# Optimization experiments

Measured on AMD Instinct MI355X. Metric: run time of the kernel, lower is better.

Reference implementation:

```python
import jax, jax.numpy as jnp
import numpy as np

B, S, D = 4, 2048, 512
H, DQK, DV = 6, 64, 64
PROJ = (DQK + DQK + DV) * H  # 1152
EPS = 1e-5


def setup_inputs() -> dict:
    key = jax.random.key(0)
    ks = jax.random.split(key, 5)
    sc = 0.05
    return {
        "x": jax.random.normal(ks[0], (B, S, D), jnp.float32),
        "Wp": jax.random.normal(ks[1], (PROJ, D), jnp.float32) * sc,
        "bp": jax.random.normal(ks[2], (PROJ,), jnp.float32) * sc,
        "Wo": jax.random.normal(ks[3], (D, H * DV), jnp.float32) * sc,
        "bo": jax.random.normal(ks[4], (D,), jnp.float32) * sc,
        "gamma": jnp.ones((D,), jnp.float32),
        "beta": jnp.zeros((D,), jnp.float32),
    }


def reference(x, Wp, bp, Wo, bo, gamma, beta):
    b, s, d = x.shape
    # 1x1 Conv1d projection == pointwise linear: [b,s,d] @ [d,proj] -> [b,s,proj]
    proj = jnp.einsum("bsd,pd->bsp", x, Wp) + bp
    q, k, v = proj[..., : H * DQK], proj[..., H * DQK : 2 * H * DQK], proj[..., 2 * H * DQK :]
    # split heads -> [b,h,s,depth]
    q = q.reshape(b, s, H, DQK).transpose(0, 2, 1, 3)
    k = k.reshape(b, s, H, DQK).transpose(0, 2, 1, 3)
    v = v.reshape(b, s, H, DV).transpose(0, 2, 1, 3)
    scores = jnp.einsum("bhqd,bhkd->bhqk", q, k) / jnp.sqrt(jnp.float32(DQK))
    attn = jax.nn.softmax(scores, axis=-1)  # softmax over kv axis
    out = jnp.einsum("bhqk,bhkd->bhqd", attn, v)
    # concat heads -> [b,s,h*dv]
    concat = out.transpose(0, 2, 1, 3).reshape(b, s, H * DV)
    y = jnp.einsum("bsf,df->bsd", concat, Wo) + bo
    z = x + y
    mu = jnp.mean(z, axis=-1, keepdims=True)
    var = jnp.mean(jnp.square(z - mu), axis=-1, keepdims=True)
    return (z - mu) / jnp.sqrt(var + EPS) * gamma + beta
```

## Files before the change

### kernel.cpp

```cpp
#include <hip/hip_runtime.h>

typedef __bf16 bf16;
typedef __bf16 bf16x8 __attribute__((ext_vector_type(8)));
typedef __bf16 bf16x4 __attribute__((ext_vector_type(4)));
typedef float  f32x4  __attribute__((ext_vector_type(4)));

#define BB 4
#define SS 2048
#define DD 512
#define HH 6
#define DH 64
#define PROJ 1152
#define FF 384
#define LDK 72

__device__ __forceinline__ bool probe_fp32(const unsigned* p) {
    return p[0] == 0x3F800000u;
}

__device__ __forceinline__ float fast_exp2(float x) {
#if __has_builtin(__builtin_amdgcn_exp2f)
    return __builtin_amdgcn_exp2f(x);
#else
    return __expf(x * 0.69314718f);
#endif
}

struct CvtSrcs { const void* s[7]; };

#define CB0 524288
#define CB1 598016
#define CB2 622592
#define CB3 622736
#define CB4 622800
#define CB5 622864
#define CB6 622928

__global__ __launch_bounds__(256) void cvt_all_kernel(
    CvtSrcs srcs, bf16* __restrict__ dst, const unsigned* __restrict__ probe)
{
    const int t = blockIdx.x * 256 + threadIdx.x;
    if (t >= CB6) return;
    int seg, base;
    if      (t < CB0) { seg = 0; base = 0;   }
    else if (t < CB1) { seg = 1; base = CB0; }
    else if (t < CB2) { seg = 2; base = CB1; }
    else if (t < CB3) { seg = 3; base = CB2; }
    else if (t < CB4) { seg = 4; base = CB3; }
    else if (t < CB5) { seg = 5; base = CB4; }
    else              { seg = 6; base = CB5; }
    const int li = (t - base) * 8;
    if (probe_fp32(probe)) {
        const float* s = (const float*)srcs.s[seg] + li;
        bf16x8 o;
#pragma unroll
        for (int j = 0; j < 8; ++j) o[j] = (bf16)s[j];
        *(bf16x8*)&dst[(size_t)t * 8] = o;
    } else {
        *(bf16x8*)&dst[(size_t)t * 8] =
            *(const bf16x8*)((const bf16*)srcs.s[seg] + li);
    }
}

template<int MERGE>
__global__ __launch_bounds__(256) void gemm_bt_kernel(
    const bf16* __restrict__ A, const float* __restrict__ lpart,
    const bf16* __restrict__ B, const bf16* __restrict__ bias,
    bf16* __restrict__ Cout, int M, int N, int K)
{
    __shared__ __attribute__((aligned(16))) bf16 sA[64 * LDK];
    __shared__ __attribute__((aligned(16))) bf16 sB[128 * LDK];

    const int tid  = threadIdx.x;
    const int lane = tid & 63;
    const int wave = tid >> 6;
    const int wn = wave * 32;
    const int l15 = lane & 15;
    const int quad = lane >> 4;
    const int bm = blockIdx.x * 64;
    const int bn = blockIdx.y * 128;
    const int KT = K / 64;

    int srowA[2], srowB[4];
    const int scol = (tid & 7) << 3;
#pragma unroll
    for (int j = 0; j < 2; ++j) srowA[j] = (j * 256 + tid) >> 3;
#pragma unroll
    for (int j = 0; j < 4; ++j) srowB[j] = (j * 256 + tid) >> 3;

    const bf16* pA[2]; const bf16* pB[4];
    const float* pl0[2];
#pragma unroll
    for (int j = 0; j < 2; ++j) {
        if (MERGE) {
            int row = bm + srowA[j];
            int b = row >> 11, q = row & (SS - 1);
            pA[j]  = A + ((size_t)(b * HH) * SS + q) * DH + scol;
            pl0[j] = lpart + (size_t)(b * HH) * SS + q;
        } else {
            pA[j] = A + (size_t)(bm + srowA[j]) * K + scol;
        }
    }
#pragma unroll
    for (int j = 0; j < 4; ++j)
        pB[j] = B + (size_t)(bn + srowB[j]) * K + scol;

    bf16x8 arb[2], a1b[2], brb[4];
    float l0[2], l1[2];

    auto loadAB = [&]() {
#pragma unroll
        for (int j = 0; j < 2; ++j) {
            arb[j] = *(const bf16x8*)pA[j];
            if (MERGE) {
                a1b[j] = *(const bf16x8*)(pA[j] + (size_t)BB * HH * SS * DH);
                l0[j] = pl0[j][0];
                l1[j] = pl0[j][(size_t)BB * HH * SS];
                pA[j]  += (size_t)SS * DH;
                pl0[j] += SS;
            } else {
                pA[j] += 64;
            }
        }
#pragma unroll
        for (int j = 0; j < 4; ++j) {
            brb[j] = *(const bf16x8*)pB[j];
            pB[j] += 64;
        }
    };

    loadAB();

    const f32x4 fzero = {0.f, 0.f, 0.f, 0.f};
    f32x4 acc[4][2];
#pragma unroll
    for (int mi = 0; mi < 4; ++mi)
#pragma unroll
        for (int ni = 0; ni < 2; ++ni) acc[mi][ni] = fzero;

    for (int kt = 0; kt < KT; ++kt) {
        __syncthreads();
#pragma unroll
        for (int j = 0; j < 2; ++j) {
            if (MERGE) {
                float inv = 1.f / (l0[j] + l1[j]);
                bf16x8 m;
#pragma unroll
                for (int e = 0; e < 8; ++e)
                    m[e] = (bf16)(((float)arb[j][e] + (float)a1b[j][e]) * inv);
                *(bf16x8*)&sA[srowA[j] * LDK + scol] = m;
            } else {
                *(bf16x8*)&sA[srowA[j] * LDK + scol] = arb[j];
            }
        }
#pragma unroll
        for (int j = 0; j < 4; ++j)
            *(bf16x8*)&sB[srowB[j] * LDK + scol] = brb[j];
        __syncthreads();
        if (kt + 1 < KT) loadAB();

#pragma unroll
        for (int kk = 0; kk < 2; ++kk) {
            bf16x8 af[4], bfr[2];
#pragma unroll
            for (int i = 0; i < 4; ++i)
                af[i] = *(const bf16x8*)&sA[(i * 16 + l15) * LDK + kk * 32 + quad * 8];
#pragma unroll
            for (int i = 0; i < 2; ++i)
                bfr[i] = *(const bf16x8*)&sB[(wn + i * 16 + l15) * LDK + kk * 32 + quad * 8];
#pragma unroll
            for (int mi = 0; mi < 4; ++mi)
#pragma unroll
                for (int ni = 0; ni < 2; ++ni)
                    acc[mi][ni] = __builtin_amdgcn_mfma_f32_16x16x32_bf16(
                        af[mi], bfr[ni], acc[mi][ni], 0, 0, 0);
        }
    }

#pragma unroll
    for (int mi = 0; mi < 4; ++mi) {
        int row = bm + mi * 16 + quad * 4;
#pragma unroll
        for (int ni = 0; ni < 2; ++ni) {
            int col = bn + wn + ni * 16 + l15;
            float bv = (float)bias[col];
#pragma unroll
            for (int r = 0; r < 4; ++r)
                Cout[(size_t)(row + r) * N + col] = (bf16)(acc[mi][ni][r] + bv);
        }
    }
}

__global__ __launch_bounds__(256) void vt_kernel(
    const bf16* __restrict__ proj, bf16* __restrict__ Vt)
{
    __shared__ __attribute__((aligned(16))) bf16 lt[64 * LDK];

    const int tid = threadIdx.x;
    const int s0 = blockIdx.x * 64;
    const int bh = blockIdx.y;
    const int b = bh / HH, h = bh % HH;

#pragma unroll
    for (int i = 0; i < 2; ++i) {
        int vid = i * 256 + tid;
        int sl = vid >> 3;
        int dc = (vid & 7) << 3;
        bf16x8 v = *(const bf16x8*)&proj[
            (size_t)(b * SS + s0 + sl) * PROJ + 2 * HH * DH + h * DH + dc];
#pragma unroll
        for (int j = 0; j < 8; ++j) {
            int d = dc + j;
            lt[d * LDK + (sl ^ (((d >> 3) & 3) * 8))] = v[j];
        }
    }
    __syncthreads();

#pragma unroll
    for (int i = 0; i < 2; ++i) {
        int vid = i * 256 + tid;
        int d = vid >> 3;
        int sc = (vid & 7) << 3;
        bf16x8 v = *(const bf16x8*)&lt[d * LDK + (sc ^ (((d >> 3) & 3) * 8))];
        *(bf16x8*)&Vt[(size_t)bh * DH * SS + (size_t)d * SS + s0 + sc] = v;
    }
}

__global__ __launch_bounds__(256) void attn_kernel(
    const bf16* __restrict__ proj, const bf16* __restrict__ Vt,
    bf16* __restrict__ Opart, float* __restrict__ lpart)
{
    __shared__ __attribute__((aligned(16))) bf16 sK [64 * LDK];
    __shared__ __attribute__((aligned(16))) bf16 sVt[64 * LDK];
    __shared__ __attribute__((aligned(16))) bf16 sP [4 * 32 * LDK];

    const int tid  = threadIdx.x;
    const int lane = tid & 63;
    const int wave = tid >> 6;
    const int l15  = lane & 15;
    const int quad = lane >> 4;

    const int bh = blockIdx.y;
    const int b = bh / HH, h = bh % HH;
    const int q0 = blockIdx.x * 128;
    const int kz = blockIdx.z;
    const bf16* base = proj + (size_t)b * SS * PROJ;
    const bf16* vtb  = Vt + (size_t)bh * DH * SS;

    const int sr = tid >> 3;
    const int sc = (tid & 7) << 3;

    const float QS = 0.18033688f;
    bf16x8 qf[2][2];
#pragma unroll
    for (int g = 0; g < 2; ++g) {
        const int qrow = q0 + wave * 32 + g * 16 + l15;
#pragma unroll
        for (int ks = 0; ks < 2; ++ks) {
            qf[ks][g] = *(const bf16x8*)&base[
                (size_t)qrow * PROJ + h * DH + ks * 32 + quad * 8];
#pragma unroll
            for (int j = 0; j < 8; ++j)
                qf[ks][g][j] = (bf16)((float)qf[ks][g][j] * QS);
        }
    }

    const f32x4 fzero = {0.f, 0.f, 0.f, 0.f};
    f32x4 lacc[2] = {fzero, fzero};
    f32x4 oacc[2][4];
#pragma unroll
    for (int g = 0; g < 2; ++g)
#pragma unroll
        for (int fi = 0; fi < 4; ++fi) oacc[g][fi] = fzero;

    bf16* pw = &sP[wave * 32 * LDK];

    const int kt0 = kz * (SS / 128);
    const int kt1 = kt0 + SS / 128;

    const bf16* pk[2]; const bf16* pv[2];
#pragma unroll
    for (int i = 0; i < 2; ++i) {
        int r = i * 32 + sr;
        pk[i] = &base[(size_t)(kt0 * 64 + r) * PROJ + HH * DH + h * DH + sc];
        pv[i] = &vtb[(size_t)r * SS + kt0 * 64 + sc];
    }
    auto loadKV = [&](bf16x8 (&kr)[2], bf16x8 (&vr)[2]) {
#pragma unroll
        for (int i = 0; i < 2; ++i) {
            kr[i] = *(const bf16x8*)pk[i];
            vr[i] = *(const bf16x8*)pv[i];
            pk[i] += (size_t)64 * PROJ;
            pv[i] += 64;
        }
    };

    bf16x8 kA[2], vA[2], kB[2], vB[2];
    loadKV(kA, vA);
    loadKV(kB, vB);

    auto tile = [&](int kt, bf16x8 (&kr)[2], bf16x8 (&vr)[2]) {
        __syncthreads();
#pragma unroll
        for (int i = 0; i < 2; ++i) {
            int r = i * 32 + sr;
            *(bf16x8*)&sK [r * LDK + sc] = kr[i];
            *(bf16x8*)&sVt[r * LDK + sc] = vr[i];
        }
        __syncthreads();
        if (kt + 2 < kt1) loadKV(kr, vr);

        f32x4 st[2][4];
#pragma unroll
        for (int mi = 0; mi < 4; ++mi) {
            bf16x8 af0 = *(const bf16x8*)&sK[(mi * 16 + l15) * LDK + quad * 8];
            bf16x8 af1 = *(const bf16x8*)&sK[(mi * 16 + l15) * LDK + 32 + quad * 8];
#pragma unroll
            for (int g = 0; g < 2; ++g) {
                st[g][mi] = __builtin_amdgcn_mfma_f32_16x16x32_bf16(
                    af0, qf[0][g], fzero, 0, 0, 0);
                st[g][mi] = __builtin_amdgcn_mfma_f32_16x16x32_bf16(
                    af1, qf[1][g], st[g][mi], 0, 0, 0);
            }
        }

#pragma unroll
        for (int g = 0; g < 2; ++g)
#pragma unroll
            for (int mi = 0; mi < 4; ++mi) {
#pragma unroll
                for (int r = 0; r < 4; ++r)
                    st[g][mi][r] = fast_exp2(st[g][mi][r]);
                lacc[g] += st[g][mi];
            }

#pragma unroll
        for (int g = 0; g < 2; ++g)
#pragma unroll
            for (int mi = 0; mi < 4; ++mi) {
                bf16x4 p4;
#pragma unroll
                for (int r = 0; r < 4; ++r) p4[r] = (bf16)st[g][mi][r];
                *(bf16x4*)&pw[(g * 16 + l15) * LDK + mi * 16 + quad * 4] = p4;
            }

#pragma unroll
        for (int ks = 0; ks < 2; ++ks) {
            bf16x8 bfrag[2];
#pragma unroll
            for (int g = 0; g < 2; ++g)
                bfrag[g] = *(const bf16x8*)&pw[(g * 16 + l15) * LDK + ks * 32 + quad * 8];
#pragma unroll
            for (int fi = 0; fi < 4; ++fi) {
                bf16x8 af = *(const bf16x8*)&sVt[(fi * 16 + l15) * LDK + ks * 32 + quad * 8];
#pragma unroll
                for (int g = 0; g < 2; ++g)
                    oacc[g][fi] = __builtin_amdgcn_mfma_f32_16x16x32_bf16(
                        af, bfrag[g], oacc[g][fi], 0, 0, 0);
            }
        }
    };

    for (int kt = kt0; kt < kt1; kt += 2) {
        tile(kt,     kA, vA);
        tile(kt + 1, kB, vB);
    }

    float l_part[2];
#pragma unroll
    for (int g = 0; g < 2; ++g) {
        l_part[g] = lacc[g][0] + lacc[g][1] + lacc[g][2] + lacc[g][3];
        l_part[g] += __shfl_xor(l_part[g], 16);
        l_part[g] += __shfl_xor(l_part[g], 32);
    }

    const size_t zoff = (size_t)(kz * BB * HH + bh) * SS;
#pragma unroll
    for (int g = 0; g < 2; ++g) {
        const int qg = q0 + wave * 32 + g * 16 + l15;
        bf16* orow = Opart + (zoff + qg) * DH;
#pragma unroll
        for (int fi = 0; fi < 4; ++fi) {
            bf16x4 o4;
#pragma unroll
            for (int r = 0; r < 4; ++r) o4[r] = (bf16)oacc[g][fi][r];
            *(bf16x4*)&orow[fi * 16 + quad * 4] = o4;
        }
    }
    if (lane < 16) {
#pragma unroll
        for (int g = 0; g < 2; ++g)
            lpart[zoff + q0 + wave * 32 + g * 16 + lane] = l_part[g];
    }
}

__global__ __launch_bounds__(256) void ln_kernel(
    const bf16* __restrict__ x, const bf16* __restrict__ y,
    const bf16* __restrict__ gamma, const bf16* __restrict__ beta,
    void* __restrict__ out, const unsigned* __restrict__ probe)
{
    const bool f32 = probe_fp32(probe);
    const int lane = threadIdx.x & 63;
    const int wave = threadIdx.x >> 6;
    const int row = blockIdx.x * 4 + wave;
    const size_t off = (size_t)row * DD + lane * 8;

    bf16x8 xv = *(const bf16x8*)&x[off];
    bf16x8 yv = *(const bf16x8*)&y[off];
    float z[8];
    float s = 0.f;
#pragma unroll
    for (int j = 0; j < 8; ++j) { z[j] = (float)xv[j] + (float)yv[j]; s += z[j]; }
#pragma unroll
    for (int m = 1; m < 64; m <<= 1) s += __shfl_xor(s, m);
    float mu = s * (1.f / DD);
    float s2 = 0.f;
#pragma unroll
    for (int j = 0; j < 8; ++j) { float d = z[j] - mu; s2 += d * d; }
#pragma unroll
    for (int m = 1; m < 64; m <<= 1) s2 += __shfl_xor(s2, m);
    float rs = rsqrtf(s2 * (1.f / DD) + 1e-5f);

    bf16x8 gm = *(const bf16x8*)&gamma[lane * 8];
    bf16x8 be = *(const bf16x8*)&beta[lane * 8];
    if (f32) {
        f32x4 o0, o1;
#pragma unroll
        for (int j = 0; j < 4; ++j) {
            o0[j] = (z[j]     - mu) * rs * (float)gm[j]     + (float)be[j];
            o1[j] = (z[j + 4] - mu) * rs * (float)gm[j + 4] + (float)be[j + 4];
        }
        *(f32x4*)&((float*)out)[off]     = o0;
        *(f32x4*)&((float*)out)[off + 4] = o1;
    } else {
        bf16x8 o;
#pragma unroll
        for (int j = 0; j < 8; ++j)
            o[j] = (bf16)((z[j] - mu) * rs * (float)gm[j] + (float)be[j]);
        *(bf16x8*)&((bf16*)out)[off] = o;
    }
}

extern "C" void kernel_launch(void* const* d_in, const int* in_sizes, int n_in,
                              void* d_out, int out_size, void* d_ws, size_t ws_size,
                              hipStream_t stream)
{
    const unsigned* probe = (const unsigned*)d_in[5];

    char* ws = (char*)d_ws;
    size_t o = 0;
    bf16* xb   = (bf16*)(ws + o); o += (size_t)BB * SS * DD * 2;
    bf16* Wpb  = (bf16*)(ws + o); o += (size_t)PROJ * DD * 2;
    bf16* Wob  = (bf16*)(ws + o); o += (size_t)DD * FF * 2;
    bf16* bpb  = (bf16*)(ws + o); o += PROJ * 2;
    bf16* bob  = (bf16*)(ws + o); o += DD * 2;
    bf16* gb   = (bf16*)(ws + o); o += DD * 2;
    bf16* bb   = (bf16*)(ws + o); o += DD * 2;
    bf16* proj   = (bf16*)(ws + o); o += (size_t)BB * SS * PROJ * 2;
    bf16* vtbuf  = (bf16*)(ws + o); o += (size_t)BB * HH * DH * SS * 2;
    bf16* Opart  = (bf16*)(ws + o); o += (size_t)2 * BB * HH * SS * DH * 2;
    float* lpart = (float*)(ws + o); o += (size_t)2 * BB * HH * SS * 4;
    bf16* ybuf = proj;

    CvtSrcs srcs;
    srcs.s[0] = d_in[0]; srcs.s[1] = d_in[1]; srcs.s[2] = d_in[3];
    srcs.s[3] = d_in[2]; srcs.s[4] = d_in[4]; srcs.s[5] = d_in[5];
    srcs.s[6] = d_in[6];
    cvt_all_kernel<<<(CB6 + 255) / 256, 256, 0, stream>>>(srcs, xb, probe);

    gemm_bt_kernel<0><<<dim3((BB * SS) / 64, PROJ / 128), 256, 0, stream>>>(
        xb, nullptr, Wpb, bpb, proj, BB * SS, PROJ, DD);
    vt_kernel<<<dim3(SS / 64, BB * HH), 256, 0, stream>>>(proj, vtbuf);
    attn_kernel<<<dim3(SS / 128, BB * HH, 2), 256, 0, stream>>>(
        proj, vtbuf, Opart, lpart);
    gemm_bt_kernel<1><<<dim3((BB * SS) / 64, DD / 128), 256, 0, stream>>>(
        Opart, lpart, Wob, bob, ybuf, BB * SS, DD, FF);
    ln_kernel<<<dim3((BB * SS) / 4), 256, 0, stream>>>(
        xb, ybuf, gb, bb, d_out, probe);
}
```

Measured before the change: 160.1 us.

## Split attention KV into four chunks, read V directly from global, swizzle LDS

Raises the KV split of the attention kernel from 2 to 4 so the grid has twice as many blocks, and extends the output-projection GEMM to sum four partial outputs and normalisers. V fragments are now read straight from global memory instead of being staged through LDS. K and P tiles use XOR-swizzled unpadded LDS layouts, and the kernel asks for 4 blocks per CU. This trades more partial-output traffic and uncoalesced V reads for higher occupancy and less LDS.

```diff
diff --git a/kernel.cpp b/kernel.cpp
--- a/kernel.cpp
+++ b/kernel.cpp
@@ -13,6 +13,7 @@
 #define PROJ 1152
 #define FF 384
 #define LDK 72
+#define NSPLIT 4
 
 __device__ __forceinline__ bool probe_fp32(const unsigned* p) {
     return p[0] == 0x3F800000u;
@@ -81,6 +82,9 @@
     const int bn = blockIdx.y * 128;
     const int KT = K / 64;
 
+    const size_t PS = (size_t)BB * HH * SS * DH;
+    const size_t LS = (size_t)BB * HH * SS;
+
     int srowA[2], srowB[4];
     const int scol = (tid & 7) << 3;
 #pragma unroll
@@ -105,20 +109,23 @@
     for (int j = 0; j < 4; ++j)
         pB[j] = B + (size_t)(bn + srowB[j]) * K + scol;
 
-    bf16x8 arb[2], a1b[2], brb[4];
-    float l0[2], l1[2];
+    bf16x8 arb[2], brb[4];
+    bf16x8 arm[2][NSPLIT];
+    float  lm[2][NSPLIT];
 
     auto loadAB = [&]() {
 #pragma unroll
         for (int j = 0; j < 2; ++j) {
-            arb[j] = *(const bf16x8*)pA[j];
             if (MERGE) {
-                a1b[j] = *(const bf16x8*)(pA[j] + (size_t)BB * HH * SS * DH);
-                l0[j] = pl0[j][0];
-                l1[j] = pl0[j][(size_t)BB * HH * SS];
+#pragma unroll
+                for (int p = 0; p < NSPLIT; ++p) {
+                    arm[j][p] = *(const bf16x8*)(pA[j] + (size_t)p * PS);
+                    lm[j][p]  = pl0[j][(size_t)p * LS];
+                }
                 pA[j]  += (size_t)SS * DH;
                 pl0[j] += SS;
             } else {
+                arb[j] = *(const bf16x8*)pA[j];
                 pA[j] += 64;
             }
         }
@@ -143,11 +150,18 @@
 #pragma unroll
         for (int j = 0; j < 2; ++j) {
             if (MERGE) {
-                float inv = 1.f / (l0[j] + l1[j]);
+                float lsum = 0.f;
+#pragma unroll
+                for (int p = 0; p < NSPLIT; ++p) lsum += lm[j][p];
+                float inv = 1.f / lsum;
                 bf16x8 m;
 #pragma unroll
-                for (int e = 0; e < 8; ++e)
-                    m[e] = (bf16)(((float)arb[j][e] + (float)a1b[j][e]) * inv);
+                for (int e = 0; e < 8; ++e) {
+                    float s = 0.f;
+#pragma unroll
+                    for (int p = 0; p < NSPLIT; ++p) s += (float)arm[j][p][e];
+                    m[e] = (bf16)(s * inv);
+                }
                 *(bf16x8*)&sA[srowA[j] * LDK + scol] = m;
             } else {
                 *(bf16x8*)&sA[srowA[j] * LDK + scol] = arb[j];
@@ -226,13 +240,12 @@
     }
 }
 
-__global__ __launch_bounds__(256) void attn_kernel(
+__global__ __launch_bounds__(256, 4) void attn_kernel(
     const bf16* __restrict__ proj, const bf16* __restrict__ Vt,
     bf16* __restrict__ Opart, float* __restrict__ lpart)
 {
-    __shared__ __attribute__((aligned(16))) bf16 sK [64 * LDK];
-    __shared__ __attribute__((aligned(16))) bf16 sVt[64 * LDK];
-    __shared__ __attribute__((aligned(16))) bf16 sP [4 * 32 * LDK];
+    __shared__ __attribute__((aligned(16))) bf16 sK[64 * 64];
+    __shared__ __attribute__((aligned(16))) bf16 sP[4 * 32 * 64];
 
     const int tid  = threadIdx.x;
     const int lane = tid & 63;
@@ -273,48 +286,47 @@
 #pragma unroll
         for (int fi = 0; fi < 4; ++fi) oacc[g][fi] = fzero;
 
-    bf16* pw = &sP[wave * 32 * LDK];
-
-    const int kt0 = kz * (SS / 128);
-    const int kt1 = kt0 + SS / 128;
-
-    const bf16* pk[2]; const bf16* pv[2];
+    bf16* pw = &sP[wave * 32 * 64];
+
+    const int TILES = SS / (64 * NSPLIT);
+    const int kt0 = kz * TILES;
+    const int kt1 = kt0 + TILES;
+
+    const bf16* pk[2];
 #pragma unroll
     for (int i = 0; i < 2; ++i) {
         int r = i * 32 + sr;
         pk[i] = &base[(size_t)(kt0 * 64 + r) * PROJ + HH * DH + h * DH + sc];
-        pv[i] = &vtb[(size_t)r * SS + kt0 * 64 + sc];
-    }
-    auto loadKV = [&](bf16x8 (&kr)[2], bf16x8 (&vr)[2]) {
+    }
+    auto loadK = [&](bf16x8 (&kr)[2]) {
 #pragma unroll
         for (int i = 0; i < 2; ++i) {
             kr[i] = *(const bf16x8*)pk[i];
-            vr[i] = *(const bf16x8*)pv[i];
             pk[i] += (size_t)64 * PROJ;
-            pv[i] += 64;
         }
     };
 
-    bf16x8 kA[2], vA[2], kB[2], vB[2];
-    loadKV(kA, vA);
-    loadKV(kB, vB);
-
-    auto tile = [&](int kt, bf16x8 (&kr)[2], bf16x8 (&vr)[2]) {
+    bf16x8 kA[2], kB[2];
+    loadK(kA);
+    loadK(kB);
+
+    auto tile = [&](int kt, bf16x8 (&kr)[2]) {
         __syncthreads();
 #pragma unroll
         for (int i = 0; i < 2; ++i) {
             int r = i * 32 + sr;
-            *(bf16x8*)&sK [r * LDK + sc] = kr[i];
-            *(bf16x8*)&sVt[r * LDK + sc] = vr[i];
+            *(bf16x8*)&sK[r * 64 + (sc ^ ((r & 7) << 3))] = kr[i];
         }
         __syncthreads();
-        if (kt + 2 < kt1) loadKV(kr, vr);
+        if (kt + 2 < kt1) loadK(kr);
 
         f32x4 st[2][4];
 #pragma unroll
         for (int mi = 0; mi < 4; ++mi) {
-            bf16x8 af0 = *(const bf16x8*)&sK[(mi * 16 + l15) * LDK + quad * 8];
-            bf16x8 af1 = *(const bf16x8*)&sK[(mi * 16 + l15) * LDK + 32 + quad * 8];
+            const int row = mi * 16 + l15;
+            const int sw = (row & 7) << 3;
+            bf16x8 af0 = *(const bf16x8*)&sK[row * 64 + ((quad * 8) ^ sw)];
+            bf16x8 af1 = *(const bf16x8*)&sK[row * 64 + ((32 + quad * 8) ^ sw)];
 #pragma unroll
             for (int g = 0; g < 2; ++g) {
                 st[g][mi] = __builtin_amdgcn_mfma_f32_16x16x32_bf16(
@@ -335,24 +347,31 @@
             }
 
 #pragma unroll
-        for (int g = 0; g < 2; ++g)
+        for (int g = 0; g < 2; ++g) {
+            const int r = g * 16 + l15;
+            const int sw = (r & 7) << 3;
 #pragma unroll
             for (int mi = 0; mi < 4; ++mi) {
                 bf16x4 p4;
 #pragma unroll
-                for (int r = 0; r < 4; ++r) p4[r] = (bf16)st[g][mi][r];
-                *(bf16x4*)&pw[(g * 16 + l15) * LDK + mi * 16 + quad * 4] = p4;
-            }
+                for (int e = 0; e < 4; ++e) p4[e] = (bf16)st[g][mi][e];
+                *(bf16x4*)&pw[r * 64 + ((mi * 16 + quad * 4) ^ sw)] = p4;
+            }
+        }
 
 #pragma unroll
         for (int ks = 0; ks < 2; ++ks) {
             bf16x8 bfrag[2];
 #pragma unroll
-            for (int g = 0; g < 2; ++g)
-                bfrag[g] = *(const bf16x8*)&pw[(g * 16 + l15) * LDK + ks * 32 + quad * 8];
+            for (int g = 0; g < 2; ++g) {
+                const int r = g * 16 + l15;
+                bfrag[g] = *(const bf16x8*)&pw[
+                    r * 64 + ((ks * 32 + quad * 8) ^ ((r & 7) << 3))];
+            }
 #pragma unroll
             for (int fi = 0; fi < 4; ++fi) {
-                bf16x8 af = *(const bf16x8*)&sVt[(fi * 16 + l15) * LDK + ks * 32 + quad * 8];
+                bf16x8 af = *(const bf16x8*)&vtb[
+                    (size_t)(fi * 16 + l15) * SS + kt * 64 + ks * 32 + quad * 8];
 #pragma unroll
                 for (int g = 0; g < 2; ++g)
                     oacc[g][fi] = __builtin_amdgcn_mfma_f32_16x16x32_bf16(
@@ -362,8 +381,8 @@
     };
 
     for (int kt = kt0; kt < kt1; kt += 2) {
-        tile(kt,     kA, vA);
-        tile(kt + 1, kB, vB);
+        tile(kt,     kA);
+        tile(kt + 1, kB);
     }
 
     float l_part[2];
@@ -458,8 +477,8 @@
     bf16* bb   = (bf16*)(ws + o); o += DD * 2;
     bf16* proj   = (bf16*)(ws + o); o += (size_t)BB * SS * PROJ * 2;
     bf16* vtbuf  = (bf16*)(ws + o); o += (size_t)BB * HH * DH * SS * 2;
-    bf16* Opart  = (bf16*)(ws + o); o += (size_t)2 * BB * HH * SS * DH * 2;
-    float* lpart = (float*)(ws + o); o += (size_t)2 * BB * HH * SS * 4;
+    bf16* Opart  = (bf16*)(ws + o); o += (size_t)NSPLIT * BB * HH * SS * DH * 2;
+    float* lpart = (float*)(ws + o); o += (size_t)NSPLIT * BB * HH * SS * 4;
     bf16* ybuf = proj;
 
     CvtSrcs srcs;
@@ -471,7 +490,7 @@
     gemm_bt_kernel<0><<<dim3((BB * SS) / 64, PROJ / 128), 256, 0, stream>>>(
         xb, nullptr, Wpb, bpb, proj, BB * SS, PROJ, DD);
     vt_kernel<<<dim3(SS / 64, BB * HH), 256, 0, stream>>>(proj, vtbuf);
-    attn_kernel<<<dim3(SS / 128, BB * HH, 2), 256, 0, stream>>>(
+    attn_kernel<<<dim3(SS / 128, BB * HH, NSPLIT), 256, 0, stream>>>(
         proj, vtbuf, Opart, lpart);
     gemm_bt_kernel<1><<<dim3((BB * SS) / 64, DD / 128), 256, 0, stream>>>(
         Opart, lpart, Wob, bob, ybuf, BB * SS, DD, FF);
```

Result: slower. 223.1 us (+39.3%).
